# Kernel tuning notes

Measured on AMD Instinct MI355X. Metric: run time of the kernel, lower is better.

Reference implementation:

```python
import jax, jax.numpy as jnp
import numpy as np
from jax import lax

# --- constants matching init_kwargs ---
NUM_SCALES = 3
LAMBDA_0, MU_0 = 1.0, 0.5
KAPPA_LAMBDA, KAPPA_MU = 2.0, 1.0
BASE_WEIGHT, GRADIENT_SCALING = 1.0, 5.0
CLAMP_MIN, CLAMP_MAX = 0.1, 10.0
SCALE_WEIGHTS = [1.0, 0.5, 0.25]
JAC_PENALTY_W = 0.1
BLUR_KSIZE, BLUR_SIGMA = 5, 1.1  # torchvision default sigma for ksize=5: 0.3*((5-1)*0.5-1)+0.8


def _resize1d_align_corners(x, axis, out_size):
    """Linear resize along one axis with align_corners=True (separable trilinear)."""
    n = x.shape[axis]
    if out_size == n:
        return x
    coords = jnp.arange(out_size, dtype=jnp.float32) * ((n - 1) / max(out_size - 1, 1))
    i0 = jnp.floor(coords).astype(jnp.int32)
    i1 = jnp.minimum(i0 + 1, n - 1)
    w = (coords - i0.astype(jnp.float32)).astype(x.dtype)
    shape = [1] * x.ndim
    shape[axis] = out_size
    w = w.reshape(shape)
    x0 = jnp.take(x, i0, axis=axis)
    x1 = jnp.take(x, i1, axis=axis)
    return x0 * (1 - w) + x1 * w


def trilinear_resize(x, out_sizes):
    # x: (B, C, X, Y, Z); align_corners=True trilinear is separable
    for ax, s in zip((-3, -2, -1), out_sizes):
        x = _resize1d_align_corners(x, ax % x.ndim, s)
    return x


def _blur_axis(x, axis, k):
    r = (BLUR_KSIZE - 1) // 2
    pad = [(0, 0)] * x.ndim
    pad[axis] = (r, r)
    xp = jnp.pad(x, pad, mode='reflect')
    n = x.shape[axis]
    out = jnp.zeros_like(x)
    for t in range(BLUR_KSIZE):
        out = out + k[t] * lax.slice_in_dim(xp, t, t + n, axis=axis)
    return out


def gaussian_blur3d(x):
    t = jnp.arange(BLUR_KSIZE, dtype=jnp.float32) - (BLUR_KSIZE - 1) / 2
    k = jnp.exp(-(t ** 2) / (2.0 * BLUR_SIGMA ** 2))
    k = (k / k.sum()).astype(x.dtype)
    for ax in (-3, -2, -1):
        x = _blur_axis(x, ax % x.ndim, k)
    return x


def jacobian_penalty(deform):
    # 3x3 Jacobian of the displacement at the center voxel via central differences
    B, _, X, Y, Z = deform.shape
    c = (X // 2, Y // 2, Z // 2)
    dx = 0.5 * (deform[:, :, c[0] + 1, c[1], c[2]] - deform[:, :, c[0] - 1, c[1], c[2]])
    dy = 0.5 * (deform[:, :, c[0], c[1] + 1, c[2]] - deform[:, :, c[0], c[1] - 1, c[2]])
    dz = 0.5 * (deform[:, :, c[0], c[1], c[2] + 1] - deform[:, :, c[0], c[1], c[2] - 1])
    J = jnp.stack([dx, dy, dz], axis=-1)  # (B, 3, 3)
    det = jnp.linalg.det(J)
    return jnp.mean(jax.nn.relu(-det))


def _loss_fwd(deformation_field, image):
    B, _, X, Y, Z = deformation_field.shape
    total = jnp.zeros((), dtype=deformation_field.dtype)
    for i in range(NUM_SCALES):
        scale = 2 ** i
        out_sizes = (X // scale, Y // scale, Z // scale)
        deform_s = trilinear_resize(deformation_field, out_sizes)
        image_s = trilinear_resize(image, out_sizes)
        img = image_s[:, 0]  # (B, x, y, z)
        gx, gy, gz = jnp.gradient(img, axis=(-3, -2, -1))
        image_gradient = jnp.sqrt(gx ** 2 + gy ** 2 + gz ** 2)
        ig_sm = gaussian_blur3d(image_gradient[None])  # (1, B, x, y, z)
        lam = jnp.clip(LAMBDA_0 + KAPPA_LAMBDA * ig_sm, CLAMP_MIN, CLAMP_MAX)
        mu = jnp.clip(MU_0 + KAPPA_MU * ig_sm, CLAMP_MIN, CLAMP_MAX)
        du = jnp.gradient(deform_s[:, 0], axis=(-3, -2, -1))
        dv = jnp.gradient(deform_s[:, 1], axis=(-3, -2, -1))
        dw = jnp.gradient(deform_s[:, 2], axis=(-3, -2, -1))
        E_xx, E_yy, E_zz = du[0], dv[1], dw[2]
        E_xy = 0.5 * (du[1] + dv[0])
        E_xz = 0.5 * (du[2] + dw[0])
        E_yz = 0.5 * (dv[2] + dw[1])
        trace_E = E_xx + E_yy + E_zz
        energy = (0.5 * lam * trace_E ** 2
                  + mu * (E_xx ** 2 + E_yy ** 2 + E_zz ** 2
                          + 2.0 * (E_xy ** 2 + E_xz ** 2 + E_yz ** 2)))
        weight = BASE_WEIGHT + GRADIENT_SCALING * ig_sm
        total = total + SCALE_WEIGHTS[i] * jnp.mean(weight * energy)
    total = total + JAC_PENALTY_W * jacobian_penalty(deformation_field)
    return total


def setup_inputs() -> dict:
    key = jax.random.key(0)
    k1, k2 = jax.random.split(key)
    deformation_field = jax.random.normal(k1, (2, 3, 160, 160, 160), dtype=jnp.float32)
    image = jax.random.uniform(k2, (2, 1, 160, 160, 160), dtype=jnp.float32)
    return {"deformation_field": deformation_field, "image": image}


def reference(deformation_field, image):
    return _loss_fwd(deformation_field, image)
```

## Files before the change

kernel.cpp:

```cpp
#include <hip/hip_runtime.h>

#define TPB 256

#define K0 0.0707663f
#define K1 0.2444606f
#define K2 0.3695462f

#define EB0 8000
#define EB1 1000
#define EB2 125
#define GB0 2000
#define GB1 250
#define GB2 32
#define BB0 2000
#define BB1 250
#define BB2 32
#define RHALF 2304000L
#define RBLK 9000

typedef float f4 __attribute__((ext_vector_type(4)));

__device__ __forceinline__ f4 ld4(const float* __restrict__ p) { return *(const f4*)p; }

__device__ __forceinline__ int rref(int i, int n) {
    return i < 0 ? -i : (i >= n ? 2 * n - 2 - i : i);
}

template <int NIN, int M>
__device__ __forceinline__ void resize_one(const float* __restrict__ in,
                                           float* __restrict__ out, long idx) {
    constexpr float ratio = (float)((NIN - 1.0) / (M - 1.0));
    int z = (int)(idx % M); long r = idx / M;
    int y = (int)(r % M);   r /= M;
    int x = (int)(r % M);   int bc = (int)(r / M);

    float cx = (float)x * ratio, cy = (float)y * ratio, cz = (float)z * ratio;
    int x0 = min((int)cx, NIN - 1), y0 = min((int)cy, NIN - 1), z0 = min((int)cz, NIN - 1);
    float wx = cx - (float)x0, wy = cy - (float)y0, wz = cz - (float)z0;
    int x1 = min(x0 + 1, NIN - 1), y1 = min(y0 + 1, NIN - 1), z1 = min(z0 + 1, NIN - 1);

    const float* p = in + (long)bc * NIN * NIN * NIN;
    constexpr long sx = (long)NIN * NIN;
#define AT(xi, yi, zi) p[(long)(xi) * sx + (long)(yi) * NIN + (zi)]
    float c00 = AT(x0, y0, z0) * (1.f - wz) + AT(x0, y0, z1) * wz;
    float c01 = AT(x0, y1, z0) * (1.f - wz) + AT(x0, y1, z1) * wz;
    float c10 = AT(x1, y0, z0) * (1.f - wz) + AT(x1, y0, z1) * wz;
    float c11 = AT(x1, y1, z0) * (1.f - wz) + AT(x1, y1, z1) * wz;
#undef AT
    float c0 = c00 * (1.f - wy) + c01 * wy;
    float c1 = c10 * (1.f - wy) + c11 * wy;
    out[idx] = c0 * (1.f - wx) + c1 * wx;
}

__device__ __forceinline__ void resize_dispatch(const float* __restrict__ D,
                                                const float* __restrict__ I,
                                                float* __restrict__ ds1, float* __restrict__ ds2,
                                                float* __restrict__ is1, float* __restrict__ is2,
                                                long idx) {
    if (idx < 3072000L) { resize_one<160, 80>(D, ds1, idx); return; }
    idx -= 3072000L;
    if (idx < 384000L) { resize_one<160, 40>(D, ds2, idx); return; }
    idx -= 384000L;
    if (idx < 1024000L) { resize_one<160, 80>(I, is1, idx); return; }
    idx -= 1024000L;
    resize_one<160, 40>(I, is2, idx);
}

__global__ __launch_bounds__(TPB)
void resize_all_kernel(const float* __restrict__ D, const float* __restrict__ I,
                       float* __restrict__ ds1, float* __restrict__ ds2,
                       float* __restrict__ is1, float* __restrict__ is2) {
    long idx = (long)blockIdx.x * TPB + threadIdx.x;
    resize_dispatch(D, I, ds1, ds2, is1, is2, idx);
    resize_dispatch(D, I, ds1, ds2, is1, is2, idx + RHALF);
}

template <int N>
__device__ __forceinline__ void gradmag_y4(const float* __restrict__ img,
                                           float* __restrict__ g, long idx) {
    constexpr int NZ4 = N / 4, NY4 = N / 4;
    constexpr long n2 = (long)N * N, n3 = n2 * N;
    int z4 = (int)(idx % NZ4); long r = idx / NZ4;
    int y4 = (int)(r % NY4); r /= NY4;
    int x = (int)(r % N); int b = (int)(r / N);
    int y0 = y4 * 4, z = z4 * 4;

    int xm = max(x - 1, 0), xp = min(x + 1, N - 1);
    float hx = (x == 0 || x == N - 1) ? 1.f : 0.5f;

    const float* base = img + (long)b * n3;
    const float* colx = base + (long)x * n2;
    float* gb = g + (long)b * n3 + (long)x * n2 + z;

    f4 Im = ld4(colx + (long)max(y0 - 1, 0) * N + z);
    f4 Ic = ld4(colx + (long)y0 * N + z);

#pragma unroll
    for (int jy = 0; jy < 4; ++jy) {
        int y = y0 + jy;
        int yp = min(y + 1, N - 1);
        float hy = (y == 0 || y == N - 1) ? 1.f : 0.5f;
        f4 Ip = ld4(colx + (long)yp * N + z);
        const float* rowy = colx + (long)y * N;
        f4 prev = (z > 0) ? ld4(rowy + z - 4) : Ic;
        f4 next = (z + 4 < N) ? ld4(rowy + z + 4) : Ic;
        f4 rxp = ld4(base + (long)xp * n2 + (long)y * N + z);
        f4 rxm = ld4(base + (long)xm * n2 + (long)y * N + z);

        f4 outv;
#pragma unroll
        for (int j = 0; j < 4; ++j) {
            float c = Ic[j];
            float zmv = (j == 0) ? prev[3] : Ic[(j == 0) ? 0 : j - 1];
            float zpv = (j == 3) ? next[0] : Ic[(j == 3) ? 3 : j + 1];
            int gz = z + j;
            float dz = (gz == 0) ? (zpv - c) : ((gz == N - 1) ? (c - zmv) : 0.5f * (zpv - zmv));
            float dx = hx * (rxp[j] - rxm[j]);
            float dy = hy * (Ip[j] - Im[j]);
            outv[j] = sqrtf(dx * dx + dy * dy + dz * dz);
        }
        *(f4*)(gb + (long)y * N) = outv;

        Im = Ic; Ic = Ip;
    }
}

__global__ __launch_bounds__(TPB)
void gradmag_all(const float* __restrict__ I0, const float* __restrict__ is1,
                 const float* __restrict__ is2, float* __restrict__ g0,
                 float* __restrict__ g1, float* __restrict__ g2) {
    int blk = blockIdx.x;
    if (blk < GB0)            gradmag_y4<160>(I0,  g0, (long)blk * TPB + threadIdx.x);
    else if (blk < GB0 + GB1) gradmag_y4<80> (is1, g1, (long)(blk - GB0) * TPB + threadIdx.x);
    else {
        long idx = (long)(blk - GB0 - GB1) * TPB + threadIdx.x;
        if (idx < 8000) gradmag_y4<40>(is2, g2, idx);
    }
}

template <int N>
__device__ __forceinline__ void blur_one(const float* __restrict__ in,
                                         float* __restrict__ out, long idx) {
    constexpr int NZ4 = N / 4, NY4 = N / 4;
    constexpr long n2 = (long)N * N, n3 = n2 * N;
    int z4 = (int)(idx % NZ4); long r = idx / NZ4;
    int y4 = (int)(r % NY4); r /= NY4;
    int x = (int)(r % N); int b = (int)(r / N);
    int y0 = y4 * 4, z = z4 * 4;

    const float K[5] = {K0, K1, K2, K1, K0};
    const float* base = in + (long)b * n3 + z;

    f4 cs[8];
#pragma unroll
    for (int jj = 0; jj < 8; ++jj) cs[jj] = (f4){0.f, 0.f, 0.f, 0.f};

#pragma unroll
    for (int i = 0; i < 5; ++i) {
        int qx = rref(x + i - 2, N);
        const float* px = base + (long)qx * n2;
#pragma unroll
        for (int jj = 0; jj < 8; ++jj) {
            int qy = rref(y0 - 2 + jj, N);
            cs[jj] += K[i] * ld4(px + (long)qy * N);
        }
    }
    float* ob = out + (long)b * n3 + (long)x * n2 + z;
#pragma unroll
    for (int k = 0; k < 4; ++k) {
        f4 o = K0 * cs[k] + K1 * cs[k + 1] + K2 * cs[k + 2] + K1 * cs[k + 3] + K0 * cs[k + 4];
        *(f4*)(ob + (long)(y0 + k) * N) = o;
    }
}

__global__ __launch_bounds__(TPB)
void blur_all(const float* __restrict__ g0, const float* __restrict__ g1,
              const float* __restrict__ g2, float* __restrict__ t0,
              float* __restrict__ t1, float* __restrict__ t2) {
    int blk = blockIdx.x;
    if (blk < BB0)            blur_one<160>(g0, t0, (long)blk * TPB + threadIdx.x);
    else if (blk < BB0 + BB1) blur_one<80> (g1, t1, (long)(blk - BB0) * TPB + threadIdx.x);
    else {
        long idx = (long)(blk - BB0 - BB1) * TPB + threadIdx.x;
        if (idx < 8000) blur_one<40>(g2, t2, idx);
    }
}

template <int N>
__device__ __forceinline__ float energy_one(const float* __restrict__ def,
                                            const float* __restrict__ igxy, long idx) {
    constexpr int NZ4 = N / 4;
    constexpr long n2 = (long)N * N, n3 = n2 * N;
    int z4 = (int)(idx % NZ4); long r = idx / NZ4;
    int y = (int)(r % N); r /= N;
    int x = (int)(r % N); int b = (int)(r / N);
    int z = z4 * 4;

    int xm = max(x - 1, 0), xp = min(x + 1, N - 1);
    int ym = max(y - 1, 0), yp = min(y + 1, N - 1);
    float hx = (x == 0 || x == N - 1) ? 1.f : 0.5f;
    float hy = (y == 0 || y == N - 1) ? 1.f : 0.5f;

    const float* base = def + (long)b * 3 * n3;
    long sp = (long)x * n2 + (long)y * N + z;

    f4 CC[3], CP[3], CN[3], RXP[3], RXM[3], RYP[3], RYM[3];
#pragma unroll
    for (int c = 0; c < 3; ++c) {
        const float* rc = base + (long)c * n3 + sp;
        CC[c] = ld4(rc);
        CP[c] = (z > 0) ? ld4(rc - 4) : CC[c];
        CN[c] = (z + 4 < N) ? ld4(rc + 4) : CC[c];
        RXP[c] = ld4(base + (long)c * n3 + (long)xp * n2 + (long)y * N + z);
        RXM[c] = ld4(base + (long)c * n3 + (long)xm * n2 + (long)y * N + z);
        RYP[c] = ld4(base + (long)c * n3 + (long)x * n2 + (long)yp * N + z);
        RYM[c] = ld4(base + (long)c * n3 + (long)x * n2 + (long)ym * N + z);
    }

    const float* growc = igxy + (long)b * n3 + (long)x * n2 + (long)y * N;
    f4 gcur = ld4(growc + z);
    f4 gprev, gnext;
    if (z >= 4) gprev = ld4(growc + z - 4);
    else { gprev[0] = growc[4]; gprev[1] = growc[3]; gprev[2] = growc[2]; gprev[3] = growc[1]; }
    if (z + 8 <= N) gnext = ld4(growc + z + 4);
    else { gnext[0] = growc[N - 2]; gnext[1] = growc[N - 3]; gnext[2] = growc[N - 4]; gnext[3] = growc[N - 5]; }
    float gw[12];
#pragma unroll
    for (int i = 0; i < 4; ++i) { gw[i] = gprev[i]; gw[4 + i] = gcur[i]; gw[8 + i] = gnext[i]; }

    float lsum = 0.f;
#pragma unroll
    for (int j = 0; j < 4; ++j) {
        int gz = z + j;
        float dX[3], dY[3], dZ[3];
#pragma unroll
        for (int c = 0; c < 3; ++c) {
            float cc = CC[c][j];
            float zmv = (j == 0) ? CP[c][3] : CC[c][(j == 0) ? 0 : j - 1];
            float zpv = (j == 3) ? CN[c][0] : CC[c][(j == 3) ? 3 : j + 1];
            dZ[c] = (gz == 0) ? (zpv - cc)
                              : ((gz == N - 1) ? (cc - zmv) : 0.5f * (zpv - zmv));
            dX[c] = hx * (RXP[c][j] - RXM[c][j]);
            dY[c] = hy * (RYP[c][j] - RYM[c][j]);
        }
        float igv = K0 * gw[2 + j] + K1 * gw[3 + j] + K2 * gw[4 + j]
                  + K1 * gw[5 + j] + K0 * gw[6 + j];
        float lam = fminf(fmaxf(1.0f + 2.0f * igv, 0.1f), 10.0f);
        float mu  = fminf(fmaxf(0.5f + 1.0f * igv, 0.1f), 10.0f);
        float wt  = 1.0f + 5.0f * igv;

        float Exx = dX[0], Eyy = dY[1], Ezz = dZ[2];
        float Exy = 0.5f * (dY[0] + dX[1]);
        float Exz = 0.5f * (dZ[0] + dX[2]);
        float Eyz = 0.5f * (dZ[1] + dY[2]);
        float tr = Exx + Eyy + Ezz;
        float e = 0.5f * lam * tr * tr +
                  mu * (Exx * Exx + Eyy * Eyy + Ezz * Ezz +
                        2.0f * (Exy * Exy + Exz * Exz + Eyz * Eyz));
        lsum += wt * e;
    }
    return lsum;
}

__global__ __launch_bounds__(TPB)
void energy_all(const float* __restrict__ D, const float* __restrict__ ds1,
                const float* __restrict__ ds2, const float* __restrict__ t0,
                const float* __restrict__ t1, const float* __restrict__ t2,
                float* __restrict__ partial) {
    int blk = blockIdx.x;
    float lsum;
    if (blk < EB0)            lsum = energy_one<160>(D,   t0, (long)blk * TPB + threadIdx.x);
    else if (blk < EB0 + EB1) lsum = energy_one<80> (ds1, t1, (long)(blk - EB0) * TPB + threadIdx.x);
    else                      lsum = energy_one<40> (ds2, t2, (long)(blk - EB0 - EB1) * TPB + threadIdx.x);

    __shared__ float sm[TPB];
    sm[threadIdx.x] = lsum;
    __syncthreads();
    for (int s = TPB / 2; s > 0; s >>= 1) {
        if (threadIdx.x < s) sm[threadIdx.x] += sm[threadIdx.x + s];
        __syncthreads();
    }
    if (threadIdx.x == 0) partial[blk] = sm[0];
}

__global__ __launch_bounds__(TPB)
void finalize_kernel(const float* __restrict__ partial,
                     const float* __restrict__ def, float* __restrict__ out) {
    __shared__ float sm[TPB];
    const float wts[3] = {1.0f, 0.5f, 0.25f};
    const float invcnt[3] = {1.0f / (2.0f * 160 * 160 * 160),
                             1.0f / (2.0f * 80 * 80 * 80),
                             1.0f / (2.0f * 40 * 40 * 40)};
    const int offs[3] = {0, EB0, EB0 + EB1};
    const int cnts[3] = {EB0, EB1, EB2};
    float acc = 0.f;
    for (int s = 0; s < 3; ++s) {
        float local = 0.f;
        for (int i = threadIdx.x; i < cnts[s]; i += TPB) local += partial[offs[s] + i];
        acc += wts[s] * invcnt[s] * local;
    }
    sm[threadIdx.x] = acc;
    __syncthreads();
    for (int s = TPB / 2; s > 0; s >>= 1) {
        if (threadIdx.x < s) sm[threadIdx.x] += sm[threadIdx.x + s];
        __syncthreads();
    }
    if (threadIdx.x == 0) {
        float jac = 0.f;
        const int n = 160;
        long n3 = (long)n * n * n;
        long ctr = ((long)80 * n + 80) * n + 80;
        for (int b = 0; b < 2; ++b) {
            const float* p = def + (long)b * 3 * n3;
            float J[3][3];
            for (int c = 0; c < 3; ++c) {
                const float* q = p + (long)c * n3 + ctr;
                J[c][0] = 0.5f * (q[(long)n * n] - q[-(long)n * n]);
                J[c][1] = 0.5f * (q[n] - q[-n]);
                J[c][2] = 0.5f * (q[1] - q[-1]);
            }
            float det = J[0][0] * (J[1][1] * J[2][2] - J[1][2] * J[2][1])
                      - J[0][1] * (J[1][0] * J[2][2] - J[1][2] * J[2][0])
                      + J[0][2] * (J[1][0] * J[2][1] - J[1][1] * J[2][0]);
            jac += fmaxf(-det, 0.f);
        }
        jac *= 0.5f;
        out[0] = sm[0] + 0.1f * jac;
    }
}

extern "C" void kernel_launch(void* const* d_in, const int* in_sizes, int n_in,
                              void* d_out, int out_size, void* d_ws, size_t ws_size,
                              hipStream_t stream) {
    const float* D = (const float*)d_in[0];
    const float* I = (const float*)d_in[1];
    float* out = (float*)d_out;
    float* ws = (float*)d_ws;

    const int B = 2;
    const long S0 = (long)B * 160 * 160 * 160;
    const long S1 = (long)B * 80 * 80 * 80;
    const long S2 = (long)B * 40 * 40 * 40;

    float* partials = ws;
    float* ds1 = partials + 9216;
    float* is1 = ds1 + 3 * S1;
    float* g1  = is1 + S1;
    float* t1  = g1 + S1;
    float* ds2 = t1 + S1;
    float* is2 = ds2 + 3 * S2;
    float* g2  = is2 + S2;
    float* t2  = g2 + S2;
    float* g0  = t2 + S2;
    float* t0  = g0 + S0;

    resize_all_kernel<<<RBLK, TPB, 0, stream>>>(D, I, ds1, ds2, is1, is2);
    gradmag_all<<<GB0 + GB1 + GB2, TPB, 0, stream>>>(I, is1, is2, g0, g1, g2);
    blur_all<<<BB0 + BB1 + BB2, TPB, 0, stream>>>(g0, g1, g2, t0, t1, t2);
    energy_all<<<EB0 + EB1 + EB2, TPB, 0, stream>>>(D, ds1, ds2, t0, t1, t2, partials);
    finalize_kernel<<<1, TPB, 0, stream>>>(partials, D, out);
}
```

Before: 168.9 us.

## Tile full-resolution energy pass with shared-memory halo for Y/Z neighbors

The full-resolution strain-energy branch now maps each block to a 32x32 Y-Z tile on a single x-plane. The block first stages the three displacement channels plus a Y halo and a Z halo of one float4 into LDS, then takes Y and Z neighbors from shared memory instead of issuing separate global loads. X neighbors and the blurred-gradient row are still read from global memory. This cuts redundant global traffic in the largest branch, at the cost of an extra barrier, about 16KB of LDS per block, and more complex index and boundary handling.

Measured after the change: 177.3 us. 5.0% more time.

```diff
diff --git a/kernel.cpp b/kernel.cpp
--- a/kernel.cpp
+++ b/kernel.cpp
@@ -267,13 +267,95 @@
                 const float* __restrict__ ds2, const float* __restrict__ t0,
                 const float* __restrict__ t1, const float* __restrict__ t2,
                 float* __restrict__ partial) {
+    __shared__ float dl[3][34][40];
+    __shared__ float sm[TPB];
     int blk = blockIdx.x;
-    float lsum;
-    if (blk < EB0)            lsum = energy_one<160>(D,   t0, (long)blk * TPB + threadIdx.x);
-    else if (blk < EB0 + EB1) lsum = energy_one<80> (ds1, t1, (long)(blk - EB0) * TPB + threadIdx.x);
-    else                      lsum = energy_one<40> (ds2, t2, (long)(blk - EB0 - EB1) * TPB + threadIdx.x);
-
-    __shared__ float sm[TPB];
+    float lsum = 0.f;
+
+    if (blk < EB0) {
+        constexpr int N = 160;
+        constexpr long n2 = (long)N * N, n3 = n2 * N;
+        int tz = blk % 5; int r = blk / 5;
+        int ty = r % 5; r /= 5;
+        int x = r % N; int b = r / N;
+        int Y0 = ty * 32, Z0 = tz * 32;
+
+        const float* db = D + (long)b * 3 * n3 + (long)x * n2;
+        for (int i = threadIdx.x; i < 1020; i += TPB) {
+            int ch = i / 340; int rem = i - ch * 340;
+            int yy = rem / 10; int s = rem - yy * 10;
+            int gy = min(max(Y0 - 1 + yy, 0), N - 1);
+            int gz = min(max(Z0 - 4 + 4 * s, 0), N - 4);
+            *(f4*)&dl[ch][yy][4 * s] = ld4(db + (long)ch * n3 + (long)gy * N + gz);
+        }
+        __syncthreads();
+
+        int ly = threadIdx.x >> 3, lz4 = threadIdx.x & 7;
+        int y = Y0 + ly, z = Z0 + lz4 * 4;
+        int xm = max(x - 1, 0), xp = min(x + 1, N - 1);
+        float hx = (x == 0 || x == N - 1) ? 1.f : 0.5f;
+        float hy = (y == 0 || y == N - 1) ? 1.f : 0.5f;
+        const float* base = D + (long)b * 3 * n3;
+
+        f4 CC[3], CP[3], CN[3], RYP[3], RYM[3], RXP[3], RXM[3];
+#pragma unroll
+        for (int c = 0; c < 3; ++c) {
+            CC[c]  = *(const f4*)&dl[c][ly + 1][4 + lz4 * 4];
+            CP[c]  = *(const f4*)&dl[c][ly + 1][lz4 * 4];
+            CN[c]  = *(const f4*)&dl[c][ly + 1][8 + lz4 * 4];
+            RYM[c] = *(const f4*)&dl[c][ly][4 + lz4 * 4];
+            RYP[c] = *(const f4*)&dl[c][ly + 2][4 + lz4 * 4];
+            RXP[c] = ld4(base + (long)c * n3 + (long)xp * n2 + (long)y * N + z);
+            RXM[c] = ld4(base + (long)c * n3 + (long)xm * n2 + (long)y * N + z);
+        }
+
+        const float* growc = t0 + (long)b * n3 + (long)x * n2 + (long)y * N;
+        f4 gcur = ld4(growc + z);
+        f4 gprev, gnext;
+        if (z >= 4) gprev = ld4(growc + z - 4);
+        else { gprev[0] = growc[4]; gprev[1] = growc[3]; gprev[2] = growc[2]; gprev[3] = growc[1]; }
+        if (z + 8 <= N) gnext = ld4(growc + z + 4);
+        else { gnext[0] = growc[N - 2]; gnext[1] = growc[N - 3]; gnext[2] = growc[N - 4]; gnext[3] = growc[N - 5]; }
+        float gw[12];
+#pragma unroll
+        for (int i = 0; i < 4; ++i) { gw[i] = gprev[i]; gw[4 + i] = gcur[i]; gw[8 + i] = gnext[i]; }
+
+#pragma unroll
+        for (int j = 0; j < 4; ++j) {
+            int gz = z + j;
+            float dX[3], dY[3], dZ[3];
+#pragma unroll
+            for (int c = 0; c < 3; ++c) {
+                float cc = CC[c][j];
+                float zmv = (j == 0) ? CP[c][3] : CC[c][(j == 0) ? 0 : j - 1];
+                float zpv = (j == 3) ? CN[c][0] : CC[c][(j == 3) ? 3 : j + 1];
+                dZ[c] = (gz == 0) ? (zpv - cc)
+                                  : ((gz == N - 1) ? (cc - zmv) : 0.5f * (zpv - zmv));
+                dX[c] = hx * (RXP[c][j] - RXM[c][j]);
+                dY[c] = hy * (RYP[c][j] - RYM[c][j]);
+            }
+            float igv = K0 * gw[2 + j] + K1 * gw[3 + j] + K2 * gw[4 + j]
+                      + K1 * gw[5 + j] + K0 * gw[6 + j];
+            float lam = fminf(fmaxf(1.0f + 2.0f * igv, 0.1f), 10.0f);
+            float mu  = fminf(fmaxf(0.5f + 1.0f * igv, 0.1f), 10.0f);
+            float wt  = 1.0f + 5.0f * igv;
+
+            float Exx = dX[0], Eyy = dY[1], Ezz = dZ[2];
+            float Exy = 0.5f * (dY[0] + dX[1]);
+            float Exz = 0.5f * (dZ[0] + dX[2]);
+            float Eyz = 0.5f * (dZ[1] + dY[2]);
+            float tr = Exx + Eyy + Ezz;
+            float e = 0.5f * lam * tr * tr +
+                      mu * (Exx * Exx + Eyy * Eyy + Ezz * Ezz +
+                            2.0f * (Exy * Exy + Exz * Exz + Eyz * Eyz));
+            lsum += wt * e;
+        }
+    } else if (blk < EB0 + EB1) {
+        lsum = energy_one<80>(ds1, t1, (long)(blk - EB0) * TPB + threadIdx.x);
+    } else {
+        lsum = energy_one<40>(ds2, t2, (long)(blk - EB0 - EB1) * TPB + threadIdx.x);
+    }
+
     sm[threadIdx.x] = lsum;
     __syncthreads();
     for (int s = TPB / 2; s > 0; s >>= 1) {
```
